# Performance work log

Measured on AMD Instinct MI355X. Metric: run time of the kernel, lower is better.

## Reference

```python
import jax, jax.numpy as jnp
import numpy as np

B, S, D = 8, 2048, 1024
N = 256          # state_dim
H = 512          # selector_hidden
E = 8            # num_experts


def murmurhash3_finalizer(token_ids):
    # Torch code works in int64 but masks to 32 bits after each multiply and
    # values stay non-negative, so it is exactly uint32 wrapping arithmetic.
    x = token_ids.astype(jnp.uint32)
    x = x ^ (x >> 16)
    x = x * jnp.uint32(2246822507)
    x = x ^ (x >> 13)
    x = x * jnp.uint32(3266489909)
    x = x ^ (x >> 16)
    return x


def setup_inputs() -> dict:
    key = jax.random.key(0)
    ks = jax.random.split(key, 7)
    scale = 0.02
    return {
        "x": jax.random.normal(ks[0], (B, S, D), dtype=jnp.float32),
        "token_ids": jax.random.randint(ks[1], (B, S), 0, 50257, dtype=jnp.int32),
        "Win": jax.random.normal(ks[2], (E, N, D), dtype=jnp.float32) * scale,      # in_proj.weight per expert
        "Wsin": jax.random.normal(ks[3], (E, H, D), dtype=jnp.float32) * scale,     # selector_in.weight
        "Wsout": jax.random.normal(ks[4], (E, 4 * N, H), dtype=jnp.float32) * scale,  # selector_out.weight
        "Wout": jax.random.normal(ks[5], (E, D, N), dtype=jnp.float32) * scale,     # out_proj.weight
        "dparam": jnp.ones((E, N), dtype=jnp.float32),                              # per-expert d
    }


def _forward(x, Win, Wsin, Wsout, Wout, dparam, token_ids):
    b, s, d = x.shape
    e_num, n, _ = Win.shape
    routes = (murmurhash3_finalizer(token_ids) % jnp.uint32(e_num)).astype(jnp.int32)  # (B,S)

    # Per-token expert projections, selected by hash route (masked accumulation
    # over the small fixed expert count; honors per-token routing).
    u = jnp.zeros((b, s, n), x.dtype)
    a = jnp.zeros((b, s, n), x.dtype)
    bg = jnp.zeros((b, s, n), x.dtype)
    c = jnp.zeros((b, s, n), x.dtype)
    dg = jnp.zeros((b, s, n), x.dtype)
    for e in range(e_num):
        m = (routes == e)[..., None]
        u = jnp.where(m, jnp.einsum('bsd,nd->bsn', x, Win[e]), u)
        sh = jax.nn.silu(jnp.einsum('bsd,hd->bsh', x, Wsin[e]))
        sel = jnp.einsum('bsh,oh->bso', sh, Wsout[e])       # (B,S,4N)
        ar, br, cr, dr = jnp.split(sel, 4, axis=-1)
        a = jnp.where(m, jax.nn.sigmoid(ar), a)
        bg = jnp.where(m, jnp.tanh(br), bg)
        c = jnp.where(m, jnp.tanh(cr), c)
        dg = jnp.where(m, jax.nn.sigmoid(dr), dg)

    dvec = dparam[routes]              # (B,S,N) expert d param per token
    skip = dvec * dg * u               # residual term, state-independent

    bidx = jnp.arange(b)

    def step(states, inp):
        # states: (B,E,N) per-expert hidden state per batch row
        route_t, u_t, a_t, b_t, c_t, skip_t = inp
        h_prev = states[bidx, route_t]                 # (B,N)
        h = a_t * h_prev + b_t * u_t
        states = states.at[bidx, route_t].set(h)       # only routed expert updates
        y = c_t * h + skip_t
        return states, y

    xs = (routes.swapaxes(0, 1), u.swapaxes(0, 1), a.swapaxes(0, 1),
          bg.swapaxes(0, 1), c.swapaxes(0, 1), skip.swapaxes(0, 1))
    states0 = jnp.zeros((b, e_num, n), x.dtype)
    _, ys = jax.lax.scan(step, states0, xs)            # ys: (S,B,N)
    y = ys.swapaxes(0, 1)                              # (B,S,N)

    out = jnp.zeros((b, s, d), x.dtype)
    for e in range(e_num):
        m = (routes == e)[..., None]
        out = jnp.where(m, jnp.einsum('bsn,dn->bsd', y, Wout[e]), out)
    return out


def reference(x, token_ids, Win, Wsin, Wsout, Wout, dparam):
    return _forward(x, Win, Wsin, Wsout, Wout, dparam, token_ids)
```

## Files before the change

kernel.cpp:

```cpp
#include <hip/hip_runtime.h>


#define TOKS 16384
#define RPAD 16512
#define DD   1024
#define NN   256
#define HH   512
#define MAXTILES  136
#define MAXCHUNKS 1088
#define CHUNK 16

typedef short short8 __attribute__((ext_vector_type(8)));
typedef float floatx4 __attribute__((ext_vector_type(4)));
typedef _Float16 half_t;

#define AS_GLOBAL __attribute__((address_space(1)))
#define AS_LDS    __attribute__((address_space(3)))

__device__ __forceinline__ void gl_lds16(const void* g, void* l) {
    __builtin_amdgcn_global_load_lds((const AS_GLOBAL void*)g, (AS_LDS void*)l, 16, 0, 0);
}

__device__ __forceinline__ unsigned short f2bf(float f) {
    union { float f; unsigned u; } c; c.f = f;
    unsigned r = c.u + 0x7FFF + ((c.u >> 16) & 1);
    return (unsigned short)(r >> 16);
}
__device__ __forceinline__ int route_of(int token) {
    unsigned x = (unsigned)token;
    x ^= x >> 16; x *= 2246822507u; x ^= x >> 13; x *= 3266489909u; x ^= x >> 16;
    return (int)(x & 7u);
}
__device__ __forceinline__ float sigm(float v) { return 1.0f / (1.0f + __expf(-v)); }
__device__ __forceinline__ float ftanh(float v) {
    float e = __expf(2.0f * v);
    return 1.0f - 2.0f / (e + 1.0f);
}

__global__ void k_route(const int* __restrict__ tok, int* __restrict__ cnt) {
    int b = blockIdx.x, tid = threadIdx.x;
    __shared__ int lc[256 * 8];
    #pragma unroll
    for (int e = 0; e < 8; e++) lc[tid * 8 + e] = 0;
    #pragma unroll
    for (int i = 0; i < 8; i++) {
        int e = route_of(tok[b * 2048 + tid * 8 + i]);
        lc[tid * 8 + e]++;
    }
    __syncthreads();
    if (tid < 8) {
        int s = 0;
        for (int t = 0; t < 256; t++) s += lc[t * 8 + tid];
        cnt[b * 8 + tid] = s;
    }
}

__global__ void k_offsets(const int* __restrict__ cnt, int* __restrict__ grpoff,
                          int* __restrict__ tileE, int* __restrict__ tileS,
                          int* __restrict__ tileR,
                          int* __restrict__ cGrp, int* __restrict__ cStart,
                          int* __restrict__ cLen, int* __restrict__ gBase,
                          int* __restrict__ meta) {
    __shared__ int sc[64], ce[8], eoff[9], etile[9], gb[65], go[64];
    int tid = threadIdx.x;
    if (tid < 64) sc[tid] = cnt[tid];
    __syncthreads();
    if (tid < 8) { int s = 0; for (int b = 0; b < 8; b++) s += sc[b * 8 + tid]; ce[tid] = s; }
    __syncthreads();
    if (tid == 0) {
        eoff[0] = 0; etile[0] = 0;
        for (int e = 0; e < 8; e++) {
            eoff[e + 1] = eoff[e] + ce[e];
            etile[e + 1] = etile[e] + (ce[e] + 127) / 128;
        }
        meta[0] = etile[8];
        gb[0] = 0;
        for (int g = 0; g < 64; g++) gb[g + 1] = gb[g] + (sc[g] + CHUNK - 1) / CHUNK;
        meta[1] = gb[64];
    }
    __syncthreads();
    if (tid < 64) {
        int b = tid >> 3, e = tid & 7;
        int run = eoff[e];
        for (int b2 = 0; b2 < b; b2++) run += sc[b2 * 8 + e];
        go[tid] = run;
        grpoff[tid] = run;
    }
    __syncthreads();
    if (tid < 8) {
        int e = tid, st = eoff[e], c = ce[e], t0 = etile[e];
        for (int i = 0, k = 0; i < c; i += 128, k++) {
            tileE[t0 + k] = e; tileS[t0 + k] = st + i;
            tileR[t0 + k] = (c - i < 128) ? (c - i) : 128;
        }
    }
    if (tid < 64) {
        int g = tid, n = sc[g], base = gb[g], s0 = go[g];
        gBase[g] = base;
        for (int i = 0, c = 0; i < n; i += CHUNK, c++) {
            cGrp[base + c] = g;
            cStart[base + c] = s0 + i;
            cLen[base + c] = (n - i < CHUNK) ? (n - i) : CHUNK;
        }
    }
}

__global__ void k_scatter(const int* __restrict__ tok, const int* __restrict__ grpoff,
                          int* __restrict__ perm) {
    int b = blockIdx.x, tid = threadIdx.x;
    __shared__ int lh[8 * 256];
    int r[8];
    int myc[8] = {0,0,0,0,0,0,0,0};
    #pragma unroll
    for (int i = 0; i < 8; i++) {
        int e = route_of(tok[b * 2048 + tid * 8 + i]);
        r[i] = e; myc[e]++;
    }
    #pragma unroll
    for (int e = 0; e < 8; e++) lh[e * 256 + tid] = myc[e];
    __syncthreads();
    for (int e = 0; e < 8; e++) {
        for (int off = 1; off < 256; off <<= 1) {
            int add = (tid >= off) ? lh[e * 256 + tid - off] : 0;
            __syncthreads();
            lh[e * 256 + tid] += add;
            __syncthreads();
        }
    }
    int basep[8];
    #pragma unroll
    for (int e = 0; e < 8; e++) basep[e] = grpoff[b * 8 + e] + lh[e * 256 + tid] - myc[e];
    #pragma unroll
    for (int i = 0; i < 8; i++) {
        int e = r[i];
        perm[basep[e]++] = b * 2048 + tid * 8 + i;
    }
}

__global__ void k_cvtw(const float* __restrict__ Win, const float* __restrict__ Wsin,
                       const float* __restrict__ Wsout, const float* __restrict__ Wout,
                       unsigned short* __restrict__ W12, unsigned short* __restrict__ Wso,
                       unsigned short* __restrict__ Wo) {
    const int C12 = 8 * 768 * 1024 / 4, CSO = 8 * 1024 * 512 / 4, CWO = 8 * 1024 * 256 / 4;
    int c = blockIdx.x * 256 + threadIdx.x;
    float4 v; unsigned short* dst;
    if (c < C12) {
        int d = c * 4;
        int e = d / (768 * 1024);
        int rem = d - e * (768 * 1024);
        int r = rem >> 10, k = rem & 1023;
        const float* src = (r < 256) ? (Win + (((size_t)e * 256 + r) << 10) + k)
                                     : (Wsin + (((size_t)e * 512 + (r - 256)) << 10) + k);
        v = *(const float4*)src;
        dst = W12 + d;
    } else if (c < C12 + CSO) {
        int d = (c - C12) * 4;
        v = *(const float4*)(Wsout + d);
        dst = Wso + d;
    } else if (c < C12 + CSO + CWO) {
        int d = (c - C12 - CSO) * 4;
        v = *(const float4*)(Wout + d);
        dst = Wo + d;
    } else return;
    ushort4 o;
    o.x = f2bf(v.x); o.y = f2bf(v.y); o.z = f2bf(v.z); o.w = f2bf(v.w);
    *(ushort4*)dst = o;
}

__global__ void k_gather(const float* __restrict__ x, const int* __restrict__ perm,
                         unsigned short* __restrict__ Xs, unsigned short* __restrict__ SHb,
                         unsigned short* __restrict__ Yb) {
    int r = blockIdx.x, t = threadIdx.x;
    if (r < TOKS) {
        int tok = perm[r];
        float4 v = *(const float4*)(x + (size_t)tok * 1024 + t * 4);
        ushort4 o;
        o.x = f2bf(v.x); o.y = f2bf(v.y); o.z = f2bf(v.z); o.w = f2bf(v.w);
        *(ushort4*)(Xs + (size_t)r * 1024 + t * 4) = o;
    } else {
        ushort4 z = {0, 0, 0, 0};
        *(ushort4*)(Xs + (size_t)r * 1024 + t * 4) = z;
        if (t < 128) *(ushort4*)(SHb + (size_t)r * 512 + t * 4) = z;
        if (t < 64)  *(ushort4*)(Yb + (size_t)r * 256 + t * 4) = z;
    }
}

template<int MODE, int KD>
__global__ __launch_bounds__(256, 3)
void k_mfma(const unsigned short* __restrict__ A, const unsigned short* __restrict__ Bw,
            const int* __restrict__ perm, const float* __restrict__ dparam,
            half_t* __restrict__ Ub, unsigned short* __restrict__ SHb,
            half_t* __restrict__ Aa, half_t* __restrict__ Wg,
            half_t* __restrict__ Cc, half_t* __restrict__ Sk,
            float* __restrict__ out,
            const int* __restrict__ tileE, const int* __restrict__ tileS,
            const int* __restrict__ tileR, const int* __restrict__ meta) {
    int mt = blockIdx.x;
    if (mt >= meta[0]) return;
    const int e = tileE[mt], pos0 = tileS[mt], rows = tileR[mt];
    const int col0 = blockIdx.y * 128;
    const int tid = threadIdx.x;
    const int w = tid >> 6, lane = tid & 63, quad = lane >> 4, l15 = lane & 15;
    const int wm = w & 1, wn = w >> 1;
    constexpr int NOUT = (MODE == 0) ? 768 : 1024;

    __shared__ unsigned short As[2 * 128 * 32];
    __shared__ unsigned short Bs[2 * 128 * 32];

    const int r0 = tid >> 2, c8 = (tid & 3) * 8;
    const unsigned short* ga = A + (size_t)(pos0 + r0) * KD + c8;
    const unsigned short* gb = Bw + ((size_t)e * NOUT + col0 + r0) * KD + c8;

    floatx4 acc[4][4] = {};

    int aoff[4], boff[4];
    #pragma unroll
    for (int i = 0; i < 4; i++) aoff[i] = (wm * 64 + i * 16 + l15) * 32 + quad * 8;
    #pragma unroll
    for (int j = 0; j < 4; j++) boff[j] = (wn * 64 + j * 16 + l15) * 32 + quad * 8;

    for (int k0 = 0; k0 < KD; k0 += 64) {
        __syncthreads();
        gl_lds16(ga + k0,                          As + w * 512);
        gl_lds16(ga + (size_t)64 * KD + k0,        As + 2048 + w * 512);
        gl_lds16(ga + k0 + 32,                     As + 4096 + w * 512);
        gl_lds16(ga + (size_t)64 * KD + k0 + 32,   As + 6144 + w * 512);
        gl_lds16(gb + k0,                          Bs + w * 512);
        gl_lds16(gb + (size_t)64 * KD + k0,        Bs + 2048 + w * 512);
        gl_lds16(gb + k0 + 32,                     Bs + 4096 + w * 512);
        gl_lds16(gb + (size_t)64 * KD + k0 + 32,   Bs + 6144 + w * 512);
        __syncthreads();
        #pragma unroll
        for (int kb = 0; kb < 2; kb++) {
            short8 af[4], bf[4];
            #pragma unroll
            for (int i = 0; i < 4; i++) af[i] = *(const short8*)(As + kb * 4096 + aoff[i]);
            #pragma unroll
            for (int j = 0; j < 4; j++) bf[j] = *(const short8*)(Bs + kb * 4096 + boff[j]);
            #pragma unroll
            for (int i = 0; i < 4; i++)
                #pragma unroll
                for (int j = 0; j < 4; j++)
                    acc[i][j] = __builtin_amdgcn_mfma_f32_16x16x32_bf16(af[i], bf[j], acc[i][j], 0, 0, 0);
        }
    }

    #pragma unroll
    for (int i = 0; i < 4; i++) {
        #pragma unroll
        for (int r = 0; r < 4; r++) {
            int m = wm * 64 + i * 16 + quad * 4 + r;
            if (m >= rows) continue;
            size_t row = (size_t)(pos0 + m);
            if (MODE == 0) {
                if (col0 < 256) {
                    #pragma unroll
                    for (int j = 0; j < 4; j++) {
                        int n = col0 + wn * 64 + j * 16 + l15;
                        Ub[row * 256 + n] = (half_t)acc[i][j][r];
                    }
                } else {
                    #pragma unroll
                    for (int j = 0; j < 4; j++) {
                        int n = col0 - 256 + wn * 64 + j * 16 + l15;
                        float v = acc[i][j][r];
                        SHb[row * 512 + n] = f2bf(v * sigm(v));
                    }
                }
            } else if (MODE == 1) {
                int region = col0 >> 8;
                #pragma unroll
                for (int j = 0; j < 4; j++) {
                    int n0 = (col0 & 255) + wn * 64 + j * 16 + l15;
                    size_t idx = row * 256 + (size_t)n0;
                    float v = acc[i][j][r];
                    if (region == 0) {
                        Aa[idx] = (half_t)sigm(v);
                    } else if (region == 1) {
                        Wg[idx] = (half_t)(ftanh(v) * (float)Ub[idx]);
                    } else if (region == 2) {
                        Cc[idx] = (half_t)ftanh(v);
                    } else {
                        Sk[idx] = (half_t)(dparam[e * 256 + n0] * sigm(v) * (float)Ub[idx]);
                    }
                }
            } else {
                int tok = perm[row];
                #pragma unroll
                for (int j = 0; j < 4; j++) {
                    int n = col0 + wn * 64 + j * 16 + l15;
                    out[(size_t)tok * 1024 + n] = acc[i][j][r];
                }
            }
        }
    }
}

__global__ void k_scanA(const half_t* __restrict__ Aa, const half_t* __restrict__ Wg,
                        const int* __restrict__ cStart, const int* __restrict__ cLen,
                        const int* __restrict__ meta,
                        float* __restrict__ SA, float* __restrict__ SQ) {
    int id = blockIdx.x;
    if (id >= meta[1]) return;
    int t = threadIdx.x;
    int s0 = cStart[id], L = cLen[id];
    size_t idx = (size_t)s0 * 256 + t;
    float p = 1.0f, q = 0.0f;
    for (int i = 0; i < L; i++) {
        float a = (float)Aa[idx], ww = (float)Wg[idx];
        q = a * q + ww;
        p *= a;
        idx += 256;
    }
    SA[(size_t)id * 256 + t] = p;
    SQ[(size_t)id * 256 + t] = q;
}

__global__ void k_scanB(const float* __restrict__ SA, const float* __restrict__ SQ,
                        const int* __restrict__ gBase, const int* __restrict__ cnt,
                        float* __restrict__ Hin) {
    int g = blockIdx.x, t = threadIdx.x;
    int base = gBase[g], nch = (cnt[g] + CHUNK - 1) / CHUNK;
    float h = 0.0f;
    for (int c = 0; c < nch; c++) {
        size_t k = (size_t)(base + c) * 256 + t;
        Hin[k] = h;
        h = SA[k] * h + SQ[k];
    }
}

__global__ void k_scanC(const half_t* __restrict__ Aa, const half_t* __restrict__ Wg,
                        const half_t* __restrict__ Cc, const half_t* __restrict__ Sk,
                        const int* __restrict__ cStart, const int* __restrict__ cLen,
                        const int* __restrict__ meta, const float* __restrict__ Hin,
                        unsigned short* __restrict__ Yb) {
    int id = blockIdx.x;
    if (id >= meta[1]) return;
    int t = threadIdx.x;
    int s0 = cStart[id], L = cLen[id];
    float h = Hin[(size_t)id * 256 + t];
    size_t idx = (size_t)s0 * 256 + t;
    for (int i = 0; i < L; i++) {
        float a = (float)Aa[idx], ww = (float)Wg[idx];
        float c = (float)Cc[idx], sk = (float)Sk[idx];
        h = a * h + ww;
        Yb[idx] = f2bf(c * h + sk);
        idx += 256;
    }
}

extern "C" void kernel_launch(void* const* d_in, const int* in_sizes, int n_in,
                              void* d_out, int out_size, void* d_ws, size_t ws_size,
                              hipStream_t stream) {
    const float* xin   = (const float*)d_in[0];
    const int*   tok   = (const int*)d_in[1];
    const float* Win   = (const float*)d_in[2];
    const float* Wsin  = (const float*)d_in[3];
    const float* Wsout = (const float*)d_in[4];
    const float* Wout  = (const float*)d_in[5];
    const float* dpar  = (const float*)d_in[6];
    float* out = (float*)d_out;

    size_t off = 0;
    char* base = (char*)d_ws;
    auto alloc = [&](size_t bytes) -> void* {
        void* p = base + off;
        off += (bytes + 255) & ~(size_t)255;
        return p;
    };
    half_t*         Ub  = (half_t*)alloc((size_t)RPAD * NN * 2);
    unsigned short* SHb = (unsigned short*)alloc((size_t)RPAD * HH * 2);
    unsigned short* Xs  = (unsigned short*)alloc((size_t)RPAD * DD * 2);
    unsigned short* Yb  = (unsigned short*)alloc((size_t)RPAD * NN * 2);
    half_t* Aa = (half_t*)alloc((size_t)TOKS * NN * 2);
    half_t* Wg = (half_t*)alloc((size_t)TOKS * NN * 2);
    half_t* Cc = (half_t*)alloc((size_t)TOKS * NN * 2);
    half_t* Sk = (half_t*)alloc((size_t)TOKS * NN * 2);
    unsigned short* W12 = (unsigned short*)alloc((size_t)8 * 768 * 1024 * 2);
    unsigned short* Wso = (unsigned short*)alloc((size_t)8 * 1024 * 512 * 2);
    unsigned short* Wo  = (unsigned short*)alloc((size_t)8 * 1024 * 256 * 2);
    float* SA  = (float*)alloc((size_t)MAXCHUNKS * 256 * 4);
    float* SQ  = (float*)alloc((size_t)MAXCHUNKS * 256 * 4);
    float* Hin = (float*)alloc((size_t)MAXCHUNKS * 256 * 4);
    int* perm   = (int*)alloc(TOKS * 4);
    int* cnt    = (int*)alloc(64 * 4);
    int* grpoff = (int*)alloc(64 * 4);
    int* tileE  = (int*)alloc(MAXTILES * 4);
    int* tileS  = (int*)alloc(MAXTILES * 4);
    int* tileR  = (int*)alloc(MAXTILES * 4);
    int* cGrp   = (int*)alloc(MAXCHUNKS * 4);
    int* cStart = (int*)alloc(MAXCHUNKS * 4);
    int* cLen   = (int*)alloc(MAXCHUNKS * 4);
    int* gBase  = (int*)alloc(64 * 4);
    int* meta   = (int*)alloc(16 * 4);

    k_route<<<8, 256, 0, stream>>>(tok, cnt);
    k_offsets<<<1, 256, 0, stream>>>(cnt, grpoff, tileE, tileS, tileR,
                                     cGrp, cStart, cLen, gBase, meta);
    k_scatter<<<8, 256, 0, stream>>>(tok, grpoff, perm);
    k_cvtw<<<12288, 256, 0, stream>>>(Win, Wsin, Wsout, Wout, W12, Wso, Wo);
    k_gather<<<RPAD, 256, 0, stream>>>(xin, perm, Xs, SHb, Yb);

    k_mfma<0, 1024><<<dim3(MAXTILES, 6), 256, 0, stream>>>(Xs, W12, perm, dpar,
        Ub, SHb, Aa, Wg, Cc, Sk, out, tileE, tileS, tileR, meta);
    k_mfma<1, 512><<<dim3(MAXTILES, 8), 256, 0, stream>>>(SHb, Wso, perm, dpar,
        Ub, SHb, Aa, Wg, Cc, Sk, out, tileE, tileS, tileR, meta);

    k_scanA<<<MAXCHUNKS, 256, 0, stream>>>(Aa, Wg, cStart, cLen, meta, SA, SQ);
    k_scanB<<<64, 256, 0, stream>>>(SA, SQ, gBase, cnt, Hin);
    k_scanC<<<MAXCHUNKS, 256, 0, stream>>>(Aa, Wg, Cc, Sk, cStart, cLen, meta, Hin, Yb);

    k_mfma<2, 256><<<dim3(MAXTILES, 8), 256, 0, stream>>>(Yb, Wo, perm, dpar,
        Ub, SHb, Aa, Wg, Cc, Sk, out, tileE, tileS, tileR, meta);
}
```

Baseline: 322.9 us.

## Double-buffer MFMA GEMM K-loop and batch loads in scan kernels

The GEMM main loop now uses a K-step of 32 with two LDS buffers. The next tile is prefetched with global_load_lds while MFMAs run on the current one, which removes one of the two barriers per step. Launch bounds are raised to 4 waves-per-SIMD occupancy. The scanA and scanC kernels load all 16 chunk elements up front for full chunks, so memory latency overlaps before the serial recurrence. The risks are register pressure from the full unroll plus higher occupancy, and a possible race: the prefetch is issued right after the barrier, with no wait before the reads of the current buffer.

```diff
diff --git a/kernel.cpp b/kernel.cpp
--- a/kernel.cpp
+++ b/kernel.cpp
@@ -186,7 +186,7 @@
 }
 
 template<int MODE, int KD>
-__global__ __launch_bounds__(256, 3)
+__global__ __launch_bounds__(256, 4)
 void k_mfma(const unsigned short* __restrict__ A, const unsigned short* __restrict__ Bw,
             const int* __restrict__ perm, const float* __restrict__ dparam,
             half_t* __restrict__ Ub, unsigned short* __restrict__ SHb,
@@ -219,30 +219,29 @@
     #pragma unroll
     for (int j = 0; j < 4; j++) boff[j] = (wn * 64 + j * 16 + l15) * 32 + quad * 8;
 
-    for (int k0 = 0; k0 < KD; k0 += 64) {
+    auto stage = [&](int buf, int k0) {
+        gl_lds16(ga + k0,                   As + buf * 4096 + w * 512);
+        gl_lds16(ga + (size_t)64 * KD + k0, As + buf * 4096 + 2048 + w * 512);
+        gl_lds16(gb + k0,                   Bs + buf * 4096 + w * 512);
+        gl_lds16(gb + (size_t)64 * KD + k0, Bs + buf * 4096 + 2048 + w * 512);
+    };
+
+    stage(0, 0);
+    #pragma unroll
+    for (int k0 = 0; k0 < KD; k0 += 32) {
+        const int cur = (k0 >> 5) & 1;
         __syncthreads();
-        gl_lds16(ga + k0,                          As + w * 512);
-        gl_lds16(ga + (size_t)64 * KD + k0,        As + 2048 + w * 512);
-        gl_lds16(ga + k0 + 32,                     As + 4096 + w * 512);
-        gl_lds16(ga + (size_t)64 * KD + k0 + 32,   As + 6144 + w * 512);
-        gl_lds16(gb + k0,                          Bs + w * 512);
-        gl_lds16(gb + (size_t)64 * KD + k0,        Bs + 2048 + w * 512);
-        gl_lds16(gb + k0 + 32,                     Bs + 4096 + w * 512);
-        gl_lds16(gb + (size_t)64 * KD + k0 + 32,   Bs + 6144 + w * 512);
-        __syncthreads();
-        #pragma unroll
-        for (int kb = 0; kb < 2; kb++) {
-            short8 af[4], bf[4];
+        if (k0 + 32 < KD) stage(1 - cur, k0 + 32);
+        short8 af[4], bf[4];
+        #pragma unroll
+        for (int i = 0; i < 4; i++) af[i] = *(const short8*)(As + cur * 4096 + aoff[i]);
+        #pragma unroll
+        for (int j = 0; j < 4; j++) bf[j] = *(const short8*)(Bs + cur * 4096 + boff[j]);
+        #pragma unroll
+        for (int i = 0; i < 4; i++)
             #pragma unroll
-            for (int i = 0; i < 4; i++) af[i] = *(const short8*)(As + kb * 4096 + aoff[i]);
-            #pragma unroll
-            for (int j = 0; j < 4; j++) bf[j] = *(const short8*)(Bs + kb * 4096 + boff[j]);
-            #pragma unroll
-            for (int i = 0; i < 4; i++)
-                #pragma unroll
-                for (int j = 0; j < 4; j++)
-                    acc[i][j] = __builtin_amdgcn_mfma_f32_16x16x32_bf16(af[i], bf[j], acc[i][j], 0, 0, 0);
-        }
+            for (int j = 0; j < 4; j++)
+                acc[i][j] = __builtin_amdgcn_mfma_f32_16x16x32_bf16(af[i], bf[j], acc[i][j], 0, 0, 0);
     }
 
     #pragma unroll
@@ -306,11 +305,22 @@
     int s0 = cStart[id], L = cLen[id];
     size_t idx = (size_t)s0 * 256 + t;
     float p = 1.0f, q = 0.0f;
-    for (int i = 0; i < L; i++) {
-        float a = (float)Aa[idx], ww = (float)Wg[idx];
-        q = a * q + ww;
-        p *= a;
-        idx += 256;
+    if (L == CHUNK) {
+        float av[CHUNK], wv[CHUNK];
+        #pragma unroll
+        for (int i = 0; i < CHUNK; i++) {
+            av[i] = (float)Aa[idx + (size_t)i * 256];
+            wv[i] = (float)Wg[idx + (size_t)i * 256];
+        }
+        #pragma unroll
+        for (int i = 0; i < CHUNK; i++) { q = av[i] * q + wv[i]; p *= av[i]; }
+    } else {
+        for (int i = 0; i < L; i++) {
+            float a = (float)Aa[idx], ww = (float)Wg[idx];
+            q = a * q + ww;
+            p *= a;
+            idx += 256;
+        }
     }
     SA[(size_t)id * 256 + t] = p;
     SQ[(size_t)id * 256 + t] = q;
@@ -340,12 +350,27 @@
     int s0 = cStart[id], L = cLen[id];
     float h = Hin[(size_t)id * 256 + t];
     size_t idx = (size_t)s0 * 256 + t;
-    for (int i = 0; i < L; i++) {
-        float a = (float)Aa[idx], ww = (float)Wg[idx];
-        float c = (float)Cc[idx], sk = (float)Sk[idx];
-        h = a * h + ww;
-        Yb[idx] = f2bf(c * h + sk);
-        idx += 256;
+    if (L == CHUNK) {
+        float av[CHUNK], wv[CHUNK], cv[CHUNK], sv[CHUNK];
+        #pragma unroll
+        for (int i = 0; i < CHUNK; i++) {
+            size_t k = idx + (size_t)i * 256;
+            av[i] = (float)Aa[k]; wv[i] = (float)Wg[k];
+            cv[i] = (float)Cc[k]; sv[i] = (float)Sk[k];
+        }
+        #pragma unroll
+        for (int i = 0; i < CHUNK; i++) {
+            h = av[i] * h + wv[i];
+            Yb[idx + (size_t)i * 256] = f2bf(cv[i] * h + sv[i]);
+        }
+    } else {
+        for (int i = 0; i < L; i++) {
+            float a = (float)Aa[idx], ww = (float)Wg[idx];
+            float c = (float)Cc[idx], sk = (float)Sk[idx];
+            h = a * h + ww;
+            Yb[idx] = f2bf(c * h + sk);
+            idx += 256;
+        }
     }
 }
 
```

Measured after the change: 341.9 us. 1.06x slower.
